# Performance work log

Measured on AMD Instinct MI355X. Metric: run time of the kernel, lower is better.

Reference implementation:

```python
import jax, jax.numpy as jnp
import numpy as np

N_NODES = 100000
N_EDGES = 1200000
IN_CH, HID_CH, OUT_CH = 64, 64, 32


def setup_inputs() -> dict:
    key = jax.random.key(0)
    ks = jax.random.split(key, 8)
    x = jax.random.normal(ks[0], (N_NODES, IN_CH), dtype=jnp.float32)
    edge_index = jax.random.randint(ks[1], (2, N_EDGES), 0, N_NODES, dtype=jnp.int64)
    # SAGEConv params: lin_l acts on aggregated neighbors (has bias), lin_r on root features.
    def glorot(k, fan_in, fan_out):
        s = jnp.sqrt(6.0 / (fan_in + fan_out))
        return jax.random.uniform(k, (fan_in, fan_out), jnp.float32, -s, s)
    W1_l = glorot(ks[2], IN_CH, HID_CH)
    W1_r = glorot(ks[3], IN_CH, HID_CH)
    b1 = jnp.zeros((HID_CH,), jnp.float32)
    W2_l = glorot(ks[4], HID_CH, OUT_CH)
    W2_r = glorot(ks[5], HID_CH, OUT_CH)
    b2 = jnp.zeros((OUT_CH,), jnp.float32)
    return {"x": x, "edge_index": edge_index, "W1_l": W1_l, "W1_r": W1_r,
            "b1": b1, "W2_l": W2_l, "W2_r": W2_r, "b2": b2}


def _sage_conv(h, src, dst, W_l, W_r, b):
    # gather source-node features along edges, mean-aggregate at destinations
    msg = h[src]                                               # [E, d]
    agg = jax.ops.segment_sum(msg, dst, num_segments=N_NODES)  # [N, d]
    cnt = jax.ops.segment_sum(jnp.ones((msg.shape[0],), h.dtype), dst,
                              num_segments=N_NODES)
    agg = agg / jnp.maximum(cnt, 1.0)[:, None]                 # mean (0 if no neighbors)
    return agg @ W_l + h @ W_r + b


def reference(x, edge_index, W1_l, W1_r, b1, W2_l, W2_r, b2):
    src, dst = edge_index[0], edge_index[1]
    h = _sage_conv(x, src, dst, W1_l, W1_r, b1)
    h = jax.nn.relu(h)
    # dropout is identity in eval mode
    return _sage_conv(h, src, dst, W2_l, W2_r, b2)
```

## Files before the change

### kernel.cpp

```cpp
#include <hip/hip_runtime.h>

__device__ __forceinline__ float bf2f(unsigned short u) {
    union { unsigned int i; float f; } v;
    v.i = ((unsigned int)u) << 16;
    return v.f;
}
__device__ __forceinline__ unsigned short f2bf(float f) {
    union { float f; unsigned int u; } v;
    v.f = f;
    unsigned int u = v.u;
    u += 0x7FFFu + ((u >> 16) & 1u);
    return (unsigned short)(u >> 16);
}
__device__ __forceinline__ float loadElem(const void* p, size_t i, int isb) {
    return isb ? bf2f(((const unsigned short*)p)[i]) : ((const float*)p)[i];
}
__device__ __forceinline__ void fma4(float4& a, float s, const float4& w) {
    a.x += s * w.x; a.y += s * w.y; a.z += s * w.z; a.w += s * w.w;
}
__device__ __forceinline__ float bflo(unsigned int u) {
    union { unsigned int i; float f; } v; v.i = u << 16; return v.f;
}
__device__ __forceinline__ float bfhi(unsigned int u) {
    union { unsigned int i; float f; } v; v.i = u & 0xFFFF0000u; return v.f;
}

#define CHUNK 4096
#define BSHIFT 8

__global__ void k_detect(const int* __restrict__ ei, int newords,
                         const unsigned int* __restrict__ xw, int nxw,
                         int* __restrict__ flags) {
    __shared__ int aOr;
    __shared__ int plaus;
    if (threadIdx.x == 0) { aOr = 0; plaus = 0; }
    __syncthreads();
    int v = 0;
    for (int i = 1 + 2 * (int)threadIdx.x; i < newords; i += 512) v |= ei[i];
    int pl = 0;
    for (int i = threadIdx.x; i < nxw; i += 256) {
        unsigned short lo = (unsigned short)(xw[i] & 0xFFFFu);
        float a = fabsf(bf2f(lo));
        if (a > 1e-5f && a < 100.0f) pl++;
    }
    atomicOr(&aOr, v);
    atomicAdd(&plaus, pl);
    __syncthreads();
    if (threadIdx.x == 0) {
        flags[0] = (aOr == 0) ? 1 : 0;
        flags[1] = (2 * plaus >= nxw) ? 1 : 0;
    }
}

__global__ void k_cast(const void* __restrict__ x, unsigned short* __restrict__ xb,
                       int n8, const int* __restrict__ flags) {
    int i = blockIdx.x * blockDim.x + threadIdx.x;
    if (i >= n8) return;
    if (flags[1]) {
        ((uint4*)xb)[i] = ((const uint4*)x)[i];
    } else {
        const float4* xf = (const float4*)x;
        float4 a = xf[2 * i], b = xf[2 * i + 1];
        ushort4 lo = { f2bf(a.x), f2bf(a.y), f2bf(a.z), f2bf(a.w) };
        ushort4 hi = { f2bf(b.x), f2bf(b.y), f2bf(b.z), f2bf(b.w) };
        ((ushort4*)xb)[2 * i] = lo;
        ((ushort4*)xb)[2 * i + 1] = hi;
    }
}

__global__ __launch_bounds__(256) void k_bcount(
        const int* __restrict__ ei, const int* __restrict__ flags,
        int* __restrict__ blockHist, int E, int NBUK, int nblk) {
    __shared__ int hist[512];
    int t = threadIdx.x;
    for (int i = t; i < NBUK; i += 256) hist[i] = 0;
    __syncthreads();
    int q = flags[0];
    int e0 = blockIdx.x * CHUNK, e1 = min(E, e0 + CHUNK);
    for (int e = e0 + t; e < e1; e += 256) {
        int dst = ei[((size_t)(E + e)) << q];
        atomicAdd(&hist[dst >> BSHIFT], 1);
    }
    __syncthreads();
    for (int i = t; i < NBUK; i += 256)
        blockHist[(size_t)i * nblk + blockIdx.x] = hist[i];
}

__global__ __launch_bounds__(256) void k_rowscan(
        int* __restrict__ blockHist, int* __restrict__ bukTot, int nblk) {
    __shared__ int sh[256];
    int t = threadIdx.x;
    int* row = blockHist + (size_t)blockIdx.x * nblk;
    int carry = 0;
    for (int base = 0; base < nblk; base += 256) {
        int i = base + t;
        int v = (i < nblk) ? row[i] : 0;
        sh[t] = v;
        __syncthreads();
        for (int off = 1; off < 256; off <<= 1) {
            int u = (t >= off) ? sh[t - off] : 0;
            __syncthreads();
            sh[t] += u;
            __syncthreads();
        }
        if (i < nblk) row[i] = carry + sh[t] - v;
        int tot = sh[255];
        __syncthreads();
        carry += tot;
    }
    if (t == 0) bukTot[blockIdx.x] = carry;
}

__global__ __launch_bounds__(512) void k_toto(
        const int* __restrict__ bukTot, int* __restrict__ bukOff,
        int* __restrict__ rowptr, int NBUK, int E, int N) {
    __shared__ int sh[512];
    int t = threadIdx.x;
    int v = (t < NBUK) ? bukTot[t] : 0;
    sh[t] = v;
    __syncthreads();
    for (int off = 1; off < 512; off <<= 1) {
        int u = (t >= off) ? sh[t - off] : 0;
        __syncthreads();
        sh[t] += u;
        __syncthreads();
    }
    if (t < NBUK) bukOff[t] = sh[t] - v;
    if (t == 0) { bukOff[NBUK] = E; rowptr[N] = E; }
}

__global__ __launch_bounds__(256) void k_part(
        const int* __restrict__ ei, const int* __restrict__ flags,
        const int* __restrict__ blockHist, const int* __restrict__ bukOff,
        unsigned int* __restrict__ recs, int E, int NBUK, int nblk) {
    __shared__ int cur[512];
    int t = threadIdx.x;
    for (int i = t; i < NBUK; i += 256)
        cur[i] = blockHist[(size_t)i * nblk + blockIdx.x] + bukOff[i];
    __syncthreads();
    int q = flags[0];
    int e0 = blockIdx.x * CHUNK, e1 = min(E, e0 + CHUNK);
    for (int e = e0 + t; e < e1; e += 256) {
        int dst = ei[((size_t)(E + e)) << q];
        int src = ei[((size_t)e) << q];
        int pos = atomicAdd(&cur[dst >> BSHIFT], 1);
        recs[pos] = ((unsigned int)src << BSHIFT) | (unsigned int)(dst & ((1 << BSHIFT) - 1));
    }
}

__global__ __launch_bounds__(256) void k_csr(
        const unsigned int* __restrict__ recs, const int* __restrict__ bukOff,
        int* __restrict__ rowptr, int* __restrict__ esorted, int N) {
    __shared__ int degLoc[256];
    __shared__ int offLoc[256];
    __shared__ int wcur[256];
    int t = threadIdx.x;
    int node0 = blockIdx.x << BSHIFT;
    int r0 = bukOff[blockIdx.x], r1 = bukOff[blockIdx.x + 1];
    degLoc[t] = 0;
    __syncthreads();
    for (int i = r0 + t; i < r1; i += 256)
        atomicAdd(&degLoc[recs[i] & 255], 1);
    __syncthreads();
    int v = degLoc[t];
    offLoc[t] = v;
    __syncthreads();
    for (int off = 1; off < 256; off <<= 1) {
        int u = (t >= off) ? offLoc[t - off] : 0;
        __syncthreads();
        offLoc[t] += u;
        __syncthreads();
    }
    int excl = offLoc[t] - v;
    int node = node0 + t;
    if (node < N) rowptr[node] = r0 + excl;
    wcur[t] = r0 + excl;
    __syncthreads();
    for (int i = r0 + t; i < r1; i += 256) {
        unsigned int rec = recs[i];
        int pos = atomicAdd(&wcur[rec & 255], 1);
        esorted[pos] = (int)(rec >> BSHIFT);
    }
}

template<int CHOUT, bool RELU, bool FINAL>
__global__ __launch_bounds__(256) void k_fused(
        const unsigned short* __restrict__ feat,
        const int* __restrict__ rowptr,
        const int* __restrict__ esorted,
        const void* __restrict__ Wl,
        const void* __restrict__ Wr,
        const void* __restrict__ bias,
        void* __restrict__ outp,
        int N, const int* __restrict__ flags) {
    constexpr int SA = 68;
    __shared__ float amBuf[64 * SA];
    __shared__ unsigned short wS16[64 * CHOUT];
    __shared__ float Bs[CHOUT];

    int t = threadIdx.x;
    int isb = flags[1];
    int node0 = blockIdx.x << 6;

    if (isb) {
        for (int i = t; i < (64 * CHOUT) / 8; i += 256)
            ((uint4*)wS16)[i] = ((const uint4*)Wl)[i];
    } else {
        for (int i = t; i < 64 * CHOUT; i += 256)
            wS16[i] = f2bf(((const float*)Wl)[i]);
    }
    if (t < CHOUT) Bs[t] = loadElem(bias, t, isb);

    {
        int g = t >> 4, l = t & 15;
        int gb = (t & 63) & ~15;
#pragma unroll
        for (int jj = 0; jj < 4; ++jj) {
            int nl = g + 16 * jj;
            int node = node0 + nl;
            float ax = 0.f, ay = 0.f, az = 0.f, aw = 0.f;
            float inv = 0.f;
            if (node < N) {
                int beg = rowptr[node], end = rowptr[node + 1];
                int d = end - beg;
                if (d > 0) {
                    inv = 1.0f / (float)d;
                    for (int bs = beg; bs < end; bs += 16) {
                        int cnt = min(end - bs, 16);
                        int idx = esorted[min(bs + l, end - 1)];
                        int dd = 0;
                        for (; dd + 8 <= cnt; dd += 8) {
                            int s0 = __shfl(idx, gb + dd + 0, 64);
                            int s1 = __shfl(idx, gb + dd + 1, 64);
                            int s2 = __shfl(idx, gb + dd + 2, 64);
                            int s3 = __shfl(idx, gb + dd + 3, 64);
                            int s4 = __shfl(idx, gb + dd + 4, 64);
                            int s5 = __shfl(idx, gb + dd + 5, 64);
                            int s6 = __shfl(idx, gb + dd + 6, 64);
                            int s7 = __shfl(idx, gb + dd + 7, 64);
                            ushort4 u0 = *(const ushort4*)(feat + (size_t)s0 * 64 + 4 * l);
                            ushort4 u1 = *(const ushort4*)(feat + (size_t)s1 * 64 + 4 * l);
                            ushort4 u2 = *(const ushort4*)(feat + (size_t)s2 * 64 + 4 * l);
                            ushort4 u3 = *(const ushort4*)(feat + (size_t)s3 * 64 + 4 * l);
                            ushort4 u4 = *(const ushort4*)(feat + (size_t)s4 * 64 + 4 * l);
                            ushort4 u5 = *(const ushort4*)(feat + (size_t)s5 * 64 + 4 * l);
                            ushort4 u6 = *(const ushort4*)(feat + (size_t)s6 * 64 + 4 * l);
                            ushort4 u7 = *(const ushort4*)(feat + (size_t)s7 * 64 + 4 * l);
                            ax += bf2f(u0.x) + bf2f(u1.x) + bf2f(u2.x) + bf2f(u3.x)
                                + bf2f(u4.x) + bf2f(u5.x) + bf2f(u6.x) + bf2f(u7.x);
                            ay += bf2f(u0.y) + bf2f(u1.y) + bf2f(u2.y) + bf2f(u3.y)
                                + bf2f(u4.y) + bf2f(u5.y) + bf2f(u6.y) + bf2f(u7.y);
                            az += bf2f(u0.z) + bf2f(u1.z) + bf2f(u2.z) + bf2f(u3.z)
                                + bf2f(u4.z) + bf2f(u5.z) + bf2f(u6.z) + bf2f(u7.z);
                            aw += bf2f(u0.w) + bf2f(u1.w) + bf2f(u2.w) + bf2f(u3.w)
                                + bf2f(u4.w) + bf2f(u5.w) + bf2f(u6.w) + bf2f(u7.w);
                        }
                        for (; dd + 4 <= cnt; dd += 4) {
                            int s0 = __shfl(idx, gb + dd + 0, 64);
                            int s1 = __shfl(idx, gb + dd + 1, 64);
                            int s2 = __shfl(idx, gb + dd + 2, 64);
                            int s3 = __shfl(idx, gb + dd + 3, 64);
                            ushort4 u0 = *(const ushort4*)(feat + (size_t)s0 * 64 + 4 * l);
                            ushort4 u1 = *(const ushort4*)(feat + (size_t)s1 * 64 + 4 * l);
                            ushort4 u2 = *(const ushort4*)(feat + (size_t)s2 * 64 + 4 * l);
                            ushort4 u3 = *(const ushort4*)(feat + (size_t)s3 * 64 + 4 * l);
                            ax += bf2f(u0.x) + bf2f(u1.x) + bf2f(u2.x) + bf2f(u3.x);
                            ay += bf2f(u0.y) + bf2f(u1.y) + bf2f(u2.y) + bf2f(u3.y);
                            az += bf2f(u0.z) + bf2f(u1.z) + bf2f(u2.z) + bf2f(u3.z);
                            aw += bf2f(u0.w) + bf2f(u1.w) + bf2f(u2.w) + bf2f(u3.w);
                        }
                        for (; dd < cnt; ++dd) {
                            int s = __shfl(idx, gb + dd, 64);
                            ushort4 u = *(const ushort4*)(feat + (size_t)s * 64 + 4 * l);
                            ax += bf2f(u.x); ay += bf2f(u.y);
                            az += bf2f(u.z); aw += bf2f(u.w);
                        }
                    }
                }
            }
            *(float4*)&amBuf[nl * SA + 4 * l] =
                make_float4(ax * inv, ay * inv, az * inv, aw * inv);
        }
    }
    __syncthreads();

    constexpr int CQ = CHOUT / 4;
    constexpr int NPT = CHOUT / 16;
    int cq = t % CQ, nq = t / CQ;
    float4 acc[NPT];
#pragma unroll
    for (int j = 0; j < NPT; ++j) acc[j] = make_float4(0.f, 0.f, 0.f, 0.f);

#pragma unroll 8
    for (int k = 0; k < 64; ++k) {
        uint2 wu = *(const uint2*)&wS16[k * CHOUT + 4 * cq];
        float4 w = make_float4(bflo(wu.x), bfhi(wu.x), bflo(wu.y), bfhi(wu.y));
#pragma unroll
        for (int j = 0; j < NPT; ++j)
            fma4(acc[j], amBuf[(nq * NPT + j) * SA + k], w);
    }
    __syncthreads();

    for (int i = t; i < 64 * 8; i += 256) {
        int nl = i >> 3, k0 = (i & 7) << 3;
        int gn = node0 + nl;
        float v[8];
        if (gn < N) {
            uint4 u = *(const uint4*)(feat + (size_t)gn * 64 + k0);
            v[0] = bflo(u.x); v[1] = bfhi(u.x);
            v[2] = bflo(u.y); v[3] = bfhi(u.y);
            v[4] = bflo(u.z); v[5] = bfhi(u.z);
            v[6] = bflo(u.w); v[7] = bfhi(u.w);
        } else {
#pragma unroll
            for (int j = 0; j < 8; ++j) v[j] = 0.f;
        }
#pragma unroll
        for (int j = 0; j < 8; ++j) amBuf[nl * SA + k0 + j] = v[j];
    }
    if (isb) {
        for (int i = t; i < (64 * CHOUT) / 8; i += 256)
            ((uint4*)wS16)[i] = ((const uint4*)Wr)[i];
    } else {
        for (int i = t; i < 64 * CHOUT; i += 256)
            wS16[i] = f2bf(((const float*)Wr)[i]);
    }
    __syncthreads();

#pragma unroll 8
    for (int k = 0; k < 64; ++k) {
        uint2 wu = *(const uint2*)&wS16[k * CHOUT + 4 * cq];
        float4 w = make_float4(bflo(wu.x), bfhi(wu.x), bflo(wu.y), bfhi(wu.y));
#pragma unroll
        for (int j = 0; j < NPT; ++j)
            fma4(acc[j], amBuf[(nq * NPT + j) * SA + k], w);
    }

    float4 bv = *(const float4*)&Bs[4 * cq];
#pragma unroll
    for (int j = 0; j < NPT; ++j) {
        int nl = nq * NPT + j;
        int node = node0 + nl;
        if (node >= N) continue;
        float4 r = acc[j];
        r.x += bv.x; r.y += bv.y; r.z += bv.z; r.w += bv.w;
        if (RELU) {
            r.x = fmaxf(r.x, 0.f); r.y = fmaxf(r.y, 0.f);
            r.z = fmaxf(r.z, 0.f); r.w = fmaxf(r.w, 0.f);
        }
        if (FINAL && !isb) {
            *(float4*)((float*)outp + (size_t)node * CHOUT + 4 * cq) = r;
        } else {
            ushort4 o = { f2bf(r.x), f2bf(r.y), f2bf(r.z), f2bf(r.w) };
            *(ushort4*)((unsigned short*)outp + (size_t)node * CHOUT + 4 * cq) = o;
        }
    }
}

extern "C" void kernel_launch(void* const* d_in, const int* in_sizes, int n_in,
                              void* d_out, int out_size, void* d_ws, size_t ws_size,
                              hipStream_t stream) {
    const void* x   = d_in[0];
    const int*  ei  = (const int*)d_in[1];
    const void* W1l = d_in[2];
    const void* W1r = d_in[3];
    const void* b1  = d_in[4];
    const void* W2l = d_in[5];
    const void* W2r = d_in[6];
    const void* b2  = d_in[7];

    const int N = in_sizes[0] / 64;
    const int E = in_sizes[1] / 2;
    const int NBUK = (N + (1 << BSHIFT) - 1) >> BSHIFT;
    const int nblk = (E + CHUNK - 1) / CHUNK;

    char* base = (char*)d_ws;
    size_t off = 0;
    auto alloc = [&](size_t bytes) { size_t o = off; off = (off + bytes + 255) & ~(size_t)255; return o; };
    int* flags   = (int*)(base + alloc(256));
    int* bukTot  = (int*)(base + alloc((size_t)NBUK * 4));
    int* bukOff  = (int*)(base + alloc((size_t)(NBUK + 1) * 4));
    int* rowptr  = (int*)(base + alloc((size_t)(N + 1) * 4));
    unsigned int* recs = (unsigned int*)(base + alloc((size_t)E * 4));
    int* esorted = (int*)(base + alloc((size_t)E * 4));
    unsigned short* xb = (unsigned short*)(base + alloc((size_t)N * 64 * 2));
    unsigned short* h  = (unsigned short*)(base + alloc((size_t)N * 64 * 2));
    (void)ws_size;

    int* blockHist = (int*)xb;

    const int B = 256;
    int nd = 2 * E; if (nd > 2048) nd = 2048;

    k_detect<<<1, 256, 0, stream>>>(ei, nd, (const unsigned int*)x, 512, flags);
    k_bcount<<<nblk, B, 0, stream>>>(ei, flags, blockHist, E, NBUK, nblk);
    k_rowscan<<<NBUK, B, 0, stream>>>(blockHist, bukTot, nblk);
    k_toto<<<1, 512, 0, stream>>>(bukTot, bukOff, rowptr, NBUK, E, N);
    k_part<<<nblk, B, 0, stream>>>(ei, flags, blockHist, bukOff, recs, E, NBUK, nblk);
    k_cast<<<(N * 8 + B - 1) / B, B, 0, stream>>>(x, xb, N * 8, flags);
    k_csr<<<NBUK, B, 0, stream>>>(recs, bukOff, rowptr, esorted, N);

    const int ntile = (N + 63) / 64;
    k_fused<64, true, false><<<ntile, B, 0, stream>>>(xb, rowptr, esorted,
                                                      W1l, W1r, b1, h, N, flags);
    k_fused<32, false, true><<<ntile, B, 0, stream>>>(h, rowptr, esorted,
                                                      W2l, W2r, b2, d_out, N, flags);
}
```

Measured before the change: 231.9 us.

## Gather 16-byte rows with 8 lanes per node and stage activations as bf16

The neighbor gather now uses 8 lanes per node, each loading a full 16-byte chunk of 8 bf16 features, instead of 16 lanes with 8-byte loads. Each block runs two node passes instead of four, and edges are handled in batches of 8. The aggregated means and root features are stored in shared memory as bf16 rather than fp32, which halves the LDS footprint and lets the root features be copied in without unpacking. The intent is fewer, wider memory requests and less shared-memory traffic, at the cost of rounding the aggregated mean to bf16 before the matmul, which adds precision loss.

```diff
diff --git a/kernel.cpp b/kernel.cpp
--- a/kernel.cpp
+++ b/kernel.cpp
@@ -11,6 +11,9 @@
     unsigned int u = v.u;
     u += 0x7FFFu + ((u >> 16) & 1u);
     return (unsigned short)(u >> 16);
+}
+__device__ __forceinline__ unsigned int pack2bf(float lo, float hi) {
+    return (unsigned int)f2bf(lo) | ((unsigned int)f2bf(hi) << 16);
 }
 __device__ __forceinline__ float loadElem(const void* p, size_t i, int isb) {
     return isb ? bf2f(((const unsigned short*)p)[i]) : ((const float*)p)[i];
@@ -193,8 +196,8 @@
         const void* __restrict__ bias,
         void* __restrict__ outp,
         int N, const int* __restrict__ flags) {
-    constexpr int SA = 68;
-    __shared__ float amBuf[64 * SA];
+    constexpr int SA2 = 72;
+    __shared__ __align__(16) unsigned short amB16[64 * SA2];
     __shared__ unsigned short wS16[64 * CHOUT];
     __shared__ float Bs[CHOUT];
 
@@ -212,74 +215,94 @@
     if (t < CHOUT) Bs[t] = loadElem(bias, t, isb);
 
     {
-        int g = t >> 4, l = t & 15;
-        int gb = (t & 63) & ~15;
+        int g = t >> 3, l = t & 7;
+        int gb = (t & 63) & ~7;
+        const unsigned short* fl = feat + 8 * l;
 #pragma unroll
-        for (int jj = 0; jj < 4; ++jj) {
-            int nl = g + 16 * jj;
+        for (int jj = 0; jj < 2; ++jj) {
+            int nl = g + 32 * jj;
             int node = node0 + nl;
-            float ax = 0.f, ay = 0.f, az = 0.f, aw = 0.f;
+            float a0 = 0.f, a1 = 0.f, a2 = 0.f, a3 = 0.f;
+            float a4 = 0.f, a5 = 0.f, a6 = 0.f, a7 = 0.f;
             float inv = 0.f;
             if (node < N) {
                 int beg = rowptr[node], end = rowptr[node + 1];
                 int d = end - beg;
                 if (d > 0) {
                     inv = 1.0f / (float)d;
-                    for (int bs = beg; bs < end; bs += 16) {
-                        int cnt = min(end - bs, 16);
+                    for (int bs = beg; bs < end; bs += 8) {
+                        int cnt = min(end - bs, 8);
                         int idx = esorted[min(bs + l, end - 1)];
                         int dd = 0;
-                        for (; dd + 8 <= cnt; dd += 8) {
-                            int s0 = __shfl(idx, gb + dd + 0, 64);
-                            int s1 = __shfl(idx, gb + dd + 1, 64);
-                            int s2 = __shfl(idx, gb + dd + 2, 64);
-                            int s3 = __shfl(idx, gb + dd + 3, 64);
-                            int s4 = __shfl(idx, gb + dd + 4, 64);
-                            int s5 = __shfl(idx, gb + dd + 5, 64);
-                            int s6 = __shfl(idx, gb + dd + 6, 64);
-                            int s7 = __shfl(idx, gb + dd + 7, 64);
-                            ushort4 u0 = *(const ushort4*)(feat + (size_t)s0 * 64 + 4 * l);
-                            ushort4 u1 = *(const ushort4*)(feat + (size_t)s1 * 64 + 4 * l);
-                            ushort4 u2 = *(const ushort4*)(feat + (size_t)s2 * 64 + 4 * l);
-                            ushort4 u3 = *(const ushort4*)(feat + (size_t)s3 * 64 + 4 * l);
-                            ushort4 u4 = *(const ushort4*)(feat + (size_t)s4 * 64 + 4 * l);
-                            ushort4 u5 = *(const ushort4*)(feat + (size_t)s5 * 64 + 4 * l);
-                            ushort4 u6 = *(const ushort4*)(feat + (size_t)s6 * 64 + 4 * l);
-                            ushort4 u7 = *(const ushort4*)(feat + (size_t)s7 * 64 + 4 * l);
-                            ax += bf2f(u0.x) + bf2f(u1.x) + bf2f(u2.x) + bf2f(u3.x)
-                                + bf2f(u4.x) + bf2f(u5.x) + bf2f(u6.x) + bf2f(u7.x);
-                            ay += bf2f(u0.y) + bf2f(u1.y) + bf2f(u2.y) + bf2f(u3.y)
-                                + bf2f(u4.y) + bf2f(u5.y) + bf2f(u6.y) + bf2f(u7.y);
-                            az += bf2f(u0.z) + bf2f(u1.z) + bf2f(u2.z) + bf2f(u3.z)
-                                + bf2f(u4.z) + bf2f(u5.z) + bf2f(u6.z) + bf2f(u7.z);
-                            aw += bf2f(u0.w) + bf2f(u1.w) + bf2f(u2.w) + bf2f(u3.w)
-                                + bf2f(u4.w) + bf2f(u5.w) + bf2f(u6.w) + bf2f(u7.w);
+                        if (cnt == 8) {
+                            int s0 = __shfl(idx, gb + 0, 64);
+                            int s1 = __shfl(idx, gb + 1, 64);
+                            int s2 = __shfl(idx, gb + 2, 64);
+                            int s3 = __shfl(idx, gb + 3, 64);
+                            int s4 = __shfl(idx, gb + 4, 64);
+                            int s5 = __shfl(idx, gb + 5, 64);
+                            int s6 = __shfl(idx, gb + 6, 64);
+                            int s7 = __shfl(idx, gb + 7, 64);
+                            uint4 u0 = *(const uint4*)(fl + (size_t)s0 * 64);
+                            uint4 u1 = *(const uint4*)(fl + (size_t)s1 * 64);
+                            uint4 u2 = *(const uint4*)(fl + (size_t)s2 * 64);
+                            uint4 u3 = *(const uint4*)(fl + (size_t)s3 * 64);
+                            uint4 u4 = *(const uint4*)(fl + (size_t)s4 * 64);
+                            uint4 u5 = *(const uint4*)(fl + (size_t)s5 * 64);
+                            uint4 u6 = *(const uint4*)(fl + (size_t)s6 * 64);
+                            uint4 u7 = *(const uint4*)(fl + (size_t)s7 * 64);
+                            a0 += bflo(u0.x) + bflo(u1.x) + bflo(u2.x) + bflo(u3.x)
+                                + bflo(u4.x) + bflo(u5.x) + bflo(u6.x) + bflo(u7.x);
+                            a1 += bfhi(u0.x) + bfhi(u1.x) + bfhi(u2.x) + bfhi(u3.x)
+                                + bfhi(u4.x) + bfhi(u5.x) + bfhi(u6.x) + bfhi(u7.x);
+                            a2 += bflo(u0.y) + bflo(u1.y) + bflo(u2.y) + bflo(u3.y)
+                                + bflo(u4.y) + bflo(u5.y) + bflo(u6.y) + bflo(u7.y);
+                            a3 += bfhi(u0.y) + bfhi(u1.y) + bfhi(u2.y) + bfhi(u3.y)
+                                + bfhi(u4.y) + bfhi(u5.y) + bfhi(u6.y) + bfhi(u7.y);
+                            a4 += bflo(u0.z) + bflo(u1.z) + bflo(u2.z) + bflo(u3.z)
+                                + bflo(u4.z) + bflo(u5.z) + bflo(u6.z) + bflo(u7.z);
+                            a5 += bfhi(u0.z) + bfhi(u1.z) + bfhi(u2.z) + bfhi(u3.z)
+                                + bfhi(u4.z) + bfhi(u5.z) + bfhi(u6.z) + bfhi(u7.z);
+                            a6 += bflo(u0.w) + bflo(u1.w) + bflo(u2.w) + bflo(u3.w)
+                                + bflo(u4.w) + bflo(u5.w) + bflo(u6.w) + bflo(u7.w);
+                            a7 += bfhi(u0.w) + bfhi(u1.w) + bfhi(u2.w) + bfhi(u3.w)
+                                + bfhi(u4.w) + bfhi(u5.w) + bfhi(u6.w) + bfhi(u7.w);
+                            dd = 8;
                         }
                         for (; dd + 4 <= cnt; dd += 4) {
                             int s0 = __shfl(idx, gb + dd + 0, 64);
                             int s1 = __shfl(idx, gb + dd + 1, 64);
                             int s2 = __shfl(idx, gb + dd + 2, 64);
                             int s3 = __shfl(idx, gb + dd + 3, 64);
-                            ushort4 u0 = *(const ushort4*)(feat + (size_t)s0 * 64 + 4 * l);
-                            ushort4 u1 = *(const ushort4*)(feat + (size_t)s1 * 64 + 4 * l);
-                            ushort4 u2 = *(const ushort4*)(feat + (size_t)s2 * 64 + 4 * l);
-                            ushort4 u3 = *(const ushort4*)(feat + (size_t)s3 * 64 + 4 * l);
-                            ax += bf2f(u0.x) + bf2f(u1.x) + bf2f(u2.x) + bf2f(u3.x);
-                            ay += bf2f(u0.y) + bf2f(u1.y) + bf2f(u2.y) + bf2f(u3.y);
-                            az += bf2f(u0.z) + bf2f(u1.z) + bf2f(u2.z) + bf2f(u3.z);
-                            aw += bf2f(u0.w) + bf2f(u1.w) + bf2f(u2.w) + bf2f(u3.w);
+                            uint4 u0 = *(const uint4*)(fl + (size_t)s0 * 64);
+                            uint4 u1 = *(const uint4*)(fl + (size_t)s1 * 64);
+                            uint4 u2 = *(const uint4*)(fl + (size_t)s2 * 64);
+                            uint4 u3 = *(const uint4*)(fl + (size_t)s3 * 64);
+                            a0 += bflo(u0.x) + bflo(u1.x) + bflo(u2.x) + bflo(u3.x);
+                            a1 += bfhi(u0.x) + bfhi(u1.x) + bfhi(u2.x) + bfhi(u3.x);
+                            a2 += bflo(u0.y) + bflo(u1.y) + bflo(u2.y) + bflo(u3.y);
+                            a3 += bfhi(u0.y) + bfhi(u1.y) + bfhi(u2.y) + bfhi(u3.y);
+                            a4 += bflo(u0.z) + bflo(u1.z) + bflo(u2.z) + bflo(u3.z);
+                            a5 += bfhi(u0.z) + bfhi(u1.z) + bfhi(u2.z) + bfhi(u3.z);
+                            a6 += bflo(u0.w) + bflo(u1.w) + bflo(u2.w) + bflo(u3.w);
+                            a7 += bfhi(u0.w) + bfhi(u1.w) + bfhi(u2.w) + bfhi(u3.w);
                         }
                         for (; dd < cnt; ++dd) {
                             int s = __shfl(idx, gb + dd, 64);
-                            ushort4 u = *(const ushort4*)(feat + (size_t)s * 64 + 4 * l);
-                            ax += bf2f(u.x); ay += bf2f(u.y);
-                            az += bf2f(u.z); aw += bf2f(u.w);
+                            uint4 u = *(const uint4*)(fl + (size_t)s * 64);
+                            a0 += bflo(u.x); a1 += bfhi(u.x);
+                            a2 += bflo(u.y); a3 += bfhi(u.y);
+                            a4 += bflo(u.z); a5 += bfhi(u.z);
+                            a6 += bflo(u.w); a7 += bfhi(u.w);
                         }
                     }
                 }
             }
-            *(float4*)&amBuf[nl * SA + 4 * l] =
-                make_float4(ax * inv, ay * inv, az * inv, aw * inv);
+            uint4 packed = make_uint4(pack2bf(a0 * inv, a1 * inv),
+                                      pack2bf(a2 * inv, a3 * inv),
+                                      pack2bf(a4 * inv, a5 * inv),
+                                      pack2bf(a6 * inv, a7 * inv));
+            *(uint4*)&amB16[nl * SA2 + 8 * l] = packed;
         }
     }
     __syncthreads();
@@ -292,31 +315,26 @@
     for (int j = 0; j < NPT; ++j) acc[j] = make_float4(0.f, 0.f, 0.f, 0.f);
 
 #pragma unroll 8
-    for (int k = 0; k < 64; ++k) {
-        uint2 wu = *(const uint2*)&wS16[k * CHOUT + 4 * cq];
-        float4 w = make_float4(bflo(wu.x), bfhi(wu.x), bflo(wu.y), bfhi(wu.y));
+    for (int k2 = 0; k2 < 32; ++k2) {
+        uint2 w0 = *(const uint2*)&wS16[(2 * k2) * CHOUT + 4 * cq];
+        uint2 w1 = *(const uint2*)&wS16[(2 * k2 + 1) * CHOUT + 4 * cq];
+        float4 wv0 = make_float4(bflo(w0.x), bfhi(w0.x), bflo(w0.y), bfhi(w0.y));
+        float4 wv1 = make_float4(bflo(w1.x), bfhi(w1.x), bflo(w1.y), bfhi(w1.y));
 #pragma unroll
-        for (int j = 0; j < NPT; ++j)
-            fma4(acc[j], amBuf[(nq * NPT + j) * SA + k], w);
+        for (int j = 0; j < NPT; ++j) {
+            unsigned int am2 = *(const unsigned int*)&amB16[(nq * NPT + j) * SA2 + 2 * k2];
+            fma4(acc[j], bflo(am2), wv0);
+            fma4(acc[j], bfhi(am2), wv1);
+        }
     }
     __syncthreads();
 
     for (int i = t; i < 64 * 8; i += 256) {
-        int nl = i >> 3, k0 = (i & 7) << 3;
+        int nl = i >> 3, c = i & 7;
         int gn = node0 + nl;
-        float v[8];
-        if (gn < N) {
-            uint4 u = *(const uint4*)(feat + (size_t)gn * 64 + k0);
-            v[0] = bflo(u.x); v[1] = bfhi(u.x);
-            v[2] = bflo(u.y); v[3] = bfhi(u.y);
-            v[4] = bflo(u.z); v[5] = bfhi(u.z);
-            v[6] = bflo(u.w); v[7] = bfhi(u.w);
-        } else {
-#pragma unroll
-            for (int j = 0; j < 8; ++j) v[j] = 0.f;
-        }
-#pragma unroll
-        for (int j = 0; j < 8; ++j) amBuf[nl * SA + k0 + j] = v[j];
+        uint4 u = make_uint4(0u, 0u, 0u, 0u);
+        if (gn < N) u = *(const uint4*)(feat + (size_t)gn * 64 + 8 * c);
+        *(uint4*)&amB16[nl * SA2 + 8 * c] = u;
     }
     if (isb) {
         for (int i = t; i < (64 * CHOUT) / 8; i += 256)
@@ -328,12 +346,17 @@
     __syncthreads();
 
 #pragma unroll 8
-    for (int k = 0; k < 64; ++k) {
-        uint2 wu = *(const uint2*)&wS16[k * CHOUT + 4 * cq];
-        float4 w = make_float4(bflo(wu.x), bfhi(wu.x), bflo(wu.y), bfhi(wu.y));
+    for (int k2 = 0; k2 < 32; ++k2) {
+        uint2 w0 = *(const uint2*)&wS16[(2 * k2) * CHOUT + 4 * cq];
+        uint2 w1 = *(const uint2*)&wS16[(2 * k2 + 1) * CHOUT + 4 * cq];
+        float4 wv0 = make_float4(bflo(w0.x), bfhi(w0.x), bflo(w0.y), bfhi(w0.y));
+        float4 wv1 = make_float4(bflo(w1.x), bfhi(w1.x), bflo(w1.y), bfhi(w1.y));
 #pragma unroll
-        for (int j = 0; j < NPT; ++j)
-            fma4(acc[j], amBuf[(nq * NPT + j) * SA + k], w);
+        for (int j = 0; j < NPT; ++j) {
+            unsigned int am2 = *(const unsigned int*)&amB16[(nq * NPT + j) * SA2 + 2 * k2];
+            fma4(acc[j], bflo(am2), wv0);
+            fma4(acc[j], bfhi(am2), wv1);
+        }
     }
 
     float4 bv = *(const float4*)&Bs[4 * cq];
```

Measured after the change: 259.6 us. 11.9% more time.
